# Kernel optimization log

Hardware: AMD Instinct MI355X
Metric: run time of the kernel (lower is better)

## Reference

```python
import jax, jax.numpy as jnp
import numpy as np

N, E, G = 50000, 600000, 50
IN_CH, HID, OUT, HEADS = 5, 64, 32, 4
BN_EPS = 1e-5


def setup_inputs() -> dict:
    key = jax.random.key(0)
    ks = jax.random.split(key, 32)

    def p(i, shape, scale=0.1):
        return jax.random.normal(ks[i], shape, dtype=jnp.float32) * scale

    inp = {
        "x": jax.random.normal(ks[0], (N, IN_CH), dtype=jnp.float32),
        "edge_index": jax.random.randint(ks[1], (2, E), 0, N),
        "batch": jnp.sort(jax.random.randint(ks[2], (N,), 0, G)),
        "enc_w": p(3, (IN_CH, HID)),
        "enc_b": jnp.zeros((HID,), jnp.float32),
    }
    dims = [(HID, HID), (HID, HID), (HID, OUT)]
    i = 4
    for l, (din, dout) in enumerate(dims):
        inp[f"w{l}"] = p(i, (din, HEADS * dout)); i += 1
        inp[f"as{l}"] = p(i, (HEADS, dout)); i += 1
        inp[f"ad{l}"] = p(i, (HEADS, dout)); i += 1
        inp[f"b{l}"] = jnp.zeros((dout,), jnp.float32)
        inp[f"g{l}"] = jnp.ones((dout,), jnp.float32)
        inp[f"be{l}"] = jnp.zeros((dout,), jnp.float32)
    for name in ("eth", "man"):
        inp[f"{name}_w1"] = p(i, (OUT, OUT // 2)); i += 1
        inp[f"{name}_b1"] = jnp.zeros((OUT // 2,), jnp.float32)
        inp[f"{name}_w2"] = p(i, (OUT // 2, 1)); i += 1
        inp[f"{name}_b2"] = jnp.zeros((1,), jnp.float32)
    return inp


def _gat(h_in, src, dst, W, a_s, a_d, bias, dout):
    # PyG GATConv, heads=HEADS, concat=False (mean over heads)
    h = (h_in @ W).reshape(N, HEADS, dout)          # [N,H,C]
    es = (h * a_s).sum(-1)                          # [N,H] src attention term
    ed = (h * a_d).sum(-1)                          # [N,H] dst attention term
    e = jax.nn.leaky_relu(es[src] + ed[dst], 0.2)   # [E,H]
    m = jax.ops.segment_max(e, dst, num_segments=N)
    ex = jnp.exp(e - m[dst])
    s = jax.ops.segment_sum(ex, dst, num_segments=N)
    alpha = ex / (s[dst] + 1e-16)                   # edge softmax per dst
    out = jax.ops.segment_sum(h[src] * alpha[..., None], dst, num_segments=N)
    return out.mean(axis=1) + bias                  # mean over heads + bias


def _bn(x, g, b):  # BatchNorm1d with batch statistics
    mu = x.mean(0)
    var = x.var(0)
    return g * (x - mu) * jax.lax.rsqrt(var + BN_EPS) + b


def _head(g, w1, b1, w2, b2):
    return jax.nn.sigmoid(jax.nn.relu(g @ w1 + b1) @ w2 + b2)


def reference(x, edge_index, batch, enc_w, enc_b,
              w0, as0, ad0, b0, g0, be0,
              w1, as1, ad1, b1, g1, be1,
              w2, as2, ad2, b2, g2, be2,
              eth_w1, eth_b1, eth_w2, eth_b2,
              man_w1, man_b1, man_w2, man_b2):
    loops = jnp.arange(N)
    src = jnp.concatenate([edge_index[0], loops])
    dst = jnp.concatenate([edge_index[1], loops])

    h = x @ enc_w + enc_b
    layers = [(w0, as0, ad0, b0, g0, be0, HID),
              (w1, as1, ad1, b1, g1, be1, HID),
              (w2, as2, ad2, b2, g2, be2, OUT)]
    for i, (W, a_s, a_d, bias, gm, bt, dout) in enumerate(layers):
        h = _gat(h, src, dst, W, a_s, a_d, bias, dout)
        h = _bn(h, gm, bt)
        if i < len(layers) - 1:
            h = jax.nn.relu(h)  # dropout is identity at inference

    ones = jnp.ones((N,), h.dtype)
    counts = jax.ops.segment_sum(ones, batch, num_segments=G)  # [G]
    gsum = jax.ops.segment_sum(h, batch, num_segments=G)
    gmean = gsum / jnp.maximum(counts, 1.0)[:, None]
    gmax = jax.ops.segment_max(h, batch, num_segments=G)
    gmax = jnp.where(counts[:, None] > 0, gmax, 0.0)
    gemb = (gmean + gmax + gsum) / 3.0

    ethics = _head(gemb, eth_w1, eth_b1, eth_w2, eth_b2)
    manip = _head(gemb, man_w1, man_b1, man_w2, man_b2)
    return h, gemb, ethics, manip
```

## Files before the change

### kernel.cpp

```cpp
#include <hip/hip_runtime.h>
#include <math.h>

constexpr int kN  = 50000;
constexpr int kE  = 600000;
constexpr int kET = 650000;
constexpr int kG  = 50;
constexpr int kH  = 4;

constexpr size_t OFF_HCUR   = 0;
constexpr size_t OFF_HNEXT  = 1600000;
constexpr size_t OFF_Z      = 4800000;
constexpr size_t OFF_ES     = 11200000;
constexpr size_t OFF_ED     = 11400000;
constexpr size_t OFF_ROWPTR = 14200000;
constexpr size_t OFF_CURSOR = 14260000;
constexpr size_t OFF_SRC    = 14320000;
constexpr size_t OFF_WT2    = 14970000;
constexpr size_t OFF_AHAT   = 15000000;
constexpr size_t OFF_BN     = 15002000;
constexpr size_t OFF_GPOOL  = 15003000;
constexpr size_t OFF_SPART  = 15008000;

constexpr int kScanBlocks = (kN + 1023) / 1024;

typedef __bf16 bf16x8 __attribute__((ext_vector_type(8)));
typedef float  f32x4  __attribute__((ext_vector_type(4)));

__device__ inline ushort f2b(float f) {
    unsigned u = __float_as_uint(f);
    return (ushort)((u + 0x7FFFu + ((u >> 16) & 1u)) >> 16);
}
__device__ inline float b2f(ushort u) {
    return __uint_as_float(((unsigned)u) << 16);
}
__device__ inline unsigned enc_f(float f) {
    unsigned b = __float_as_uint(f);
    return (b & 0x80000000u) ? ~b : (b | 0x80000000u);
}
__device__ inline float dec_f(unsigned u) {
    return __uint_as_float((u & 0x80000000u) ? (u & 0x7FFFFFFFu) : ~u);
}

__device__ inline void edge_pair(const int* __restrict__ ei, int e, int& src, int& dst) {
    if (e < kE) { src = ei[e]; dst = ei[kE + e]; }
    else        { src = e - kE; dst = e - kE; }
}

__global__ void k_hist(const int* __restrict__ ei, int* __restrict__ counts) {
    int e = blockIdx.x * blockDim.x + threadIdx.x;
    if (e >= kET) return;
    int src, dst;
    edge_pair(ei, e, src, dst);
    atomicAdd(&counts[dst], 1);
}

__global__ void __launch_bounds__(1024) k_scan_local(const int* __restrict__ counts,
                                                     int* __restrict__ rowptr,
                                                     int* __restrict__ partials) {
    int tid = threadIdx.x;
    int idx = blockIdx.x * 1024 + tid;
    int val = (idx < kN) ? counts[idx] : 0;
    int lane = tid & 63, w = tid >> 6;
    int x = val;
#pragma unroll
    for (int off = 1; off < 64; off <<= 1) {
        int t = __shfl_up(x, off);
        if (lane >= off) x += t;
    }
    __shared__ int wsum[16];
    if (lane == 63) wsum[w] = x;
    __syncthreads();
    if (w == 0 && lane < 16) {
        int y = wsum[lane];
#pragma unroll
        for (int off = 1; off < 16; off <<= 1) {
            int t = __shfl_up(y, off);
            if (lane >= off) y += t;
        }
        wsum[lane] = y;
    }
    __syncthreads();
    int incl = x + (w > 0 ? wsum[w - 1] : 0);
    if (idx < kN) rowptr[idx + 1] = incl;
    if (tid == 1023) partials[blockIdx.x] = incl;
}

__global__ void k_scan_part(int* __restrict__ partials) {
    int lane = threadIdx.x;
    int v = (lane < kScanBlocks) ? partials[lane] : 0;
    int x = v;
#pragma unroll
    for (int off = 1; off < 64; off <<= 1) {
        int t = __shfl_up(x, off);
        if (lane >= off) x += t;
    }
    if (lane < kScanBlocks) partials[lane] = x - v;
}

__global__ void __launch_bounds__(1024) k_scan_add(int* __restrict__ cursor,
                                                   int* __restrict__ rowptr,
                                                   const int* __restrict__ partials) {
    int idx = blockIdx.x * 1024 + threadIdx.x;
    if (idx >= kN) return;
    int incl = rowptr[idx + 1] + partials[blockIdx.x];
    rowptr[idx + 1] = incl;
    int val = cursor[idx];
    cursor[idx] = incl - val;
    if (idx == 0) rowptr[0] = 0;
}

__global__ void k_scatter(const int* __restrict__ ei, int* __restrict__ cursor,
                          int* __restrict__ src_csr) {
    int e = blockIdx.x * blockDim.x + threadIdx.x;
    if (e >= kET) return;
    int src, dst;
    edge_pair(ei, e, src, dst);
    int pos = atomicAdd(&cursor[dst], 1);
    src_csr[pos] = src;
}

__global__ void k_prep_all(const float* __restrict__ w0, const float* __restrict__ w1,
                           const float* __restrict__ w2, const float* __restrict__ as0,
                           const float* __restrict__ as1, const float* __restrict__ as2,
                           const float* __restrict__ ad0, const float* __restrict__ ad1,
                           const float* __restrict__ ad2, float* __restrict__ ahat,
                           ushort* __restrict__ Wt2) {
    int b = blockIdx.x;
    if (b < 3) {
        const float* W  = (b == 0) ? w0 : (b == 1) ? w1 : w2;
        const float* As = (b == 0) ? as0 : (b == 1) ? as1 : as2;
        const float* Ad = (b == 0) ? ad0 : (b == 1) ? ad1 : ad2;
        int dout = (b == 2) ? 32 : 64;
        int i = threadIdx.x;
        int h = i >> 6, k = i & 63;
        const float* wr = W + (size_t)k * (4 * dout) + h * dout;
        float s1 = 0.f, s2 = 0.f;
        for (int c = 0; c < dout; ++c) {
            float w = wr[c];
            s1 += w * As[h * dout + c];
            s2 += w * Ad[h * dout + c];
        }
        ahat[b * 512 + i] = s1;
        ahat[b * 512 + 256 + i] = s2;
    } else {
        int i = (b - 3) * 256 + threadIdx.x;
        if (i >= 40960) return;
        int l, li;
        if (i < 16384)      { l = 0; li = i; }
        else if (i < 32768) { l = 1; li = i - 16384; }
        else                { l = 2; li = i - 32768; }
        int dout = (l == 2) ? 32 : 64;
        const float* W = (l == 0) ? w0 : (l == 1) ? w1 : w2;
        int c = li >> 8, kk = li & 255;
        int h = kk >> 6, k = kk & 63;
        Wt2[l * 16384 + li] = f2b(W[(size_t)k * (4 * dout) + h * dout + c]);
    }
}

__global__ void __launch_bounds__(256) k_encoder_att(const float* __restrict__ x,
                                                     const float* __restrict__ w,
                                                     const float* __restrict__ b,
                                                     const float* __restrict__ ahat0,
                                                     ushort* __restrict__ h,
                                                     float* __restrict__ es,
                                                     float* __restrict__ ed) {
    int node = blockIdx.x * 4 + (threadIdx.x >> 6);
    int lane = threadIdx.x & 63;
    float acc = b[lane];
#pragma unroll
    for (int k = 0; k < 5; ++k) acc += x[node * 5 + k] * w[k * 64 + lane];
    h[(size_t)node * 64 + lane] = f2b(acc);

    float ps[4], pd[4];
#pragma unroll
    for (int hh = 0; hh < 4; ++hh) {
        ps[hh] = acc * ahat0[hh * 64 + lane];
        pd[hh] = acc * ahat0[256 + hh * 64 + lane];
    }
#pragma unroll
    for (int off = 1; off < 64; off <<= 1) {
#pragma unroll
        for (int hh = 0; hh < 4; ++hh) {
            ps[hh] += __shfl_xor(ps[hh], off);
            pd[hh] += __shfl_xor(pd[hh], off);
        }
    }
    if (lane == 0) {
        ((float4*)es)[node] = make_float4(ps[0], ps[1], ps[2], ps[3]);
        ((float4*)ed)[node] = make_float4(pd[0], pd[1], pd[2], pd[3]);
    }
}

__global__ void __launch_bounds__(256) k_gat(const int* __restrict__ rowptr,
                                             const int* __restrict__ srcc,
                                             const float* __restrict__ es,
                                             const float* __restrict__ ed,
                                             const ushort* __restrict__ h,
                                             ushort* __restrict__ z) {
    int wid = threadIdx.x >> 6;
    int lane = threadIdx.x & 63;
    int dst = blockIdx.x * 4 + wid;
    int start = rowptr[dst], end = rowptr[dst + 1];
    int deg = end - start;

    int e_l = lane >> 2, hh = lane & 3;
    int q = lane >> 4, c4 = lane & 15;

    float edv = ed[dst * 4 + hh];
    float acc[4][4] = {};
    float s;

    if (deg <= 16) {
        int pos = start + e_l;
        int psafe = (pos < end) ? pos : start;
        int src = srcc[psafe];
        float v = es[src * 4 + hh] + edv;
        v = (v >= 0.f) ? v : 0.2f * v;
        if (pos >= end) v = -3e38f;

        uint2 hv[4];
#pragma unroll
        for (int t = 0; t < 4; ++t) {
            int p2 = start + t * 4 + q;
            int p2s = (p2 < end) ? p2 : start;
            int s2 = srcc[p2s];
            hv[t] = *reinterpret_cast<const uint2*>(h + (size_t)s2 * 64 + c4 * 4);
        }

        float cm = v;
        cm = fmaxf(cm, __shfl_xor(cm, 4));
        cm = fmaxf(cm, __shfl_xor(cm, 8));
        cm = fmaxf(cm, __shfl_xor(cm, 16));
        cm = fmaxf(cm, __shfl_xor(cm, 32));
        float p = __expf(v - cm);
        float cs = p;
        cs += __shfl_xor(cs, 4);
        cs += __shfl_xor(cs, 8);
        cs += __shfl_xor(cs, 16);
        cs += __shfl_xor(cs, 32);
        s = cs;

#pragma unroll
        for (int t = 0; t < 4; ++t) {
            int el = t * 4 + q;
            float p0 = __shfl(p, (el << 2) | 0);
            float p1 = __shfl(p, (el << 2) | 1);
            float p2 = __shfl(p, (el << 2) | 2);
            float p3 = __shfl(p, (el << 2) | 3);
            float c0 = __uint_as_float(hv[t].x << 16);
            float c1 = __uint_as_float(hv[t].x & 0xFFFF0000u);
            float c2 = __uint_as_float(hv[t].y << 16);
            float c3 = __uint_as_float(hv[t].y & 0xFFFF0000u);
            acc[0][0] += p0 * c0; acc[0][1] += p0 * c1; acc[0][2] += p0 * c2; acc[0][3] += p0 * c3;
            acc[1][0] += p1 * c0; acc[1][1] += p1 * c1; acc[1][2] += p1 * c2; acc[1][3] += p1 * c3;
            acc[2][0] += p2 * c0; acc[2][1] += p2 * c1; acc[2][2] += p2 * c2; acc[2][3] += p2 * c3;
            acc[3][0] += p3 * c0; acc[3][1] += p3 * c1; acc[3][2] += p3 * c2; acc[3][3] += p3 * c3;
        }
    } else {
        float m = -3e38f;
        s = 0.f;
        for (int cs0 = start; cs0 < end; cs0 += 16) {
            int pos = cs0 + e_l;
            int psafe = (pos < end) ? pos : start;
            int src = srcc[psafe];
            float v = es[src * 4 + hh] + edv;
            v = (v >= 0.f) ? v : 0.2f * v;
            if (pos >= end) v = -3e38f;

            float cm = v;
            cm = fmaxf(cm, __shfl_xor(cm, 4));
            cm = fmaxf(cm, __shfl_xor(cm, 8));
            cm = fmaxf(cm, __shfl_xor(cm, 16));
            cm = fmaxf(cm, __shfl_xor(cm, 32));
            float mn = fmaxf(m, cm);
            float scale = __expf(m - mn);
            float p = __expf(v - mn);
            float cth = p;
            cth += __shfl_xor(cth, 4);
            cth += __shfl_xor(cth, 8);
            cth += __shfl_xor(cth, 16);
            cth += __shfl_xor(cth, 32);
            s = s * scale + cth;
            m = mn;

            float sc0 = __shfl(scale, 0), sc1 = __shfl(scale, 1);
            float sc2 = __shfl(scale, 2), sc3 = __shfl(scale, 3);
#pragma unroll
            for (int c = 0; c < 4; ++c) {
                acc[0][c] *= sc0; acc[1][c] *= sc1; acc[2][c] *= sc2; acc[3][c] *= sc3;
            }
#pragma unroll
            for (int t = 0; t < 4; ++t) {
                int el = t * 4 + q;
                int p2 = cs0 + el;
                int p2s = (p2 < end) ? p2 : start;
                int s2 = srcc[p2s];
                uint2 hv = *reinterpret_cast<const uint2*>(h + (size_t)s2 * 64 + c4 * 4);
                float p0 = __shfl(p, (el << 2) | 0);
                float p1 = __shfl(p, (el << 2) | 1);
                float p2f = __shfl(p, (el << 2) | 2);
                float p3 = __shfl(p, (el << 2) | 3);
                float c0 = __uint_as_float(hv.x << 16);
                float c1 = __uint_as_float(hv.x & 0xFFFF0000u);
                float c2 = __uint_as_float(hv.y << 16);
                float c3 = __uint_as_float(hv.y & 0xFFFF0000u);
                acc[0][0] += p0 * c0;  acc[0][1] += p0 * c1;  acc[0][2] += p0 * c2;  acc[0][3] += p0 * c3;
                acc[1][0] += p1 * c0;  acc[1][1] += p1 * c1;  acc[1][2] += p1 * c2;  acc[1][3] += p1 * c3;
                acc[2][0] += p2f * c0; acc[2][1] += p2f * c1; acc[2][2] += p2f * c2; acc[2][3] += p2f * c3;
                acc[3][0] += p3 * c0;  acc[3][1] += p3 * c1;  acc[3][2] += p3 * c2;  acc[3][3] += p3 * c3;
            }
        }
    }

    float myinv = 0.25f / (s + 1e-16f);
    float inv0 = __shfl(myinv, 0), inv1 = __shfl(myinv, 1);
    float inv2 = __shfl(myinv, 2), inv3 = __shfl(myinv, 3);
#pragma unroll
    for (int c = 0; c < 4; ++c) {
        acc[0][c] *= inv0; acc[1][c] *= inv1; acc[2][c] *= inv2; acc[3][c] *= inv3;
    }
#pragma unroll
    for (int j = 0; j < 4; ++j) {
#pragma unroll
        for (int c = 0; c < 4; ++c) {
            float v = acc[j][c];
            v += __shfl_xor(v, 16);
            v += __shfl_xor(v, 32);
            acc[j][c] = v;
        }
    }
    if (q == 0) {
        ushort* zr = z + (size_t)dst * 256 + c4 * 4;
#pragma unroll
        for (int j = 0; j < 4; ++j) {
            ushort4 o;
            o.x = f2b(acc[j][0]); o.y = f2b(acc[j][1]);
            o.z = f2b(acc[j][2]); o.w = f2b(acc[j][3]);
            *reinterpret_cast<ushort4*>(zr + j * 64) = o;
        }
    }
}

template <int DOUT>
__global__ void __launch_bounds__(256) k_zgemm(const ushort* __restrict__ z,
                                               const ushort* __restrict__ Wt2l,
                                               float* __restrict__ hnext,
                                               float* __restrict__ bnl) {
    constexpr int NG = DOUT / 32;
    constexpr int W = 2 * DOUT;
    __shared__ float pl[4][W];
    int tid = threadIdx.x;
    int widx = tid >> 6, lane = tid & 63;
    int wid = blockIdx.x * 4 + widx;
    int mtile = wid / NG;
    int ng = wid - mtile * NG;
    bool active = (mtile < kN / 16);
    int m0 = mtile * 16;
    int n0 = ng * 32;

    int row = lane & 15;
    int k0  = (lane >> 4) * 8;

    for (int j = tid; j < 4 * W; j += 256) (&pl[0][0])[j] = 0.f;

    f32x4 acc0 = {0.f, 0.f, 0.f, 0.f};
    f32x4 acc1 = {0.f, 0.f, 0.f, 0.f};
    if (active) {
        const ushort* za = z + (size_t)(m0 + row) * 256 + k0;
        bf16x8 a[8];
#pragma unroll
        for (int ks = 0; ks < 8; ++ks)
            a[ks] = *reinterpret_cast<const bf16x8*>(za + ks * 32);

        const ushort* wb0 = Wt2l + (size_t)(n0 + row) * 256 + k0;
        const ushort* wb1 = wb0 + 16 * 256;
#pragma unroll
        for (int ks = 0; ks < 8; ++ks) {
            bf16x8 b0 = *reinterpret_cast<const bf16x8*>(wb0 + ks * 32);
            bf16x8 b1 = *reinterpret_cast<const bf16x8*>(wb1 + ks * 32);
            acc0 = __builtin_amdgcn_mfma_f32_16x16x32_bf16(a[ks], b0, acc0, 0, 0, 0);
            acc1 = __builtin_amdgcn_mfma_f32_16x16x32_bf16(a[ks], b1, acc1, 0, 0, 0);
        }

        int col = lane & 15;
        int r0  = (lane >> 4) * 4;
#pragma unroll
        for (int r = 0; r < 4; ++r) {
            hnext[(size_t)(m0 + r0 + r) * DOUT + n0 + col]      = acc0[r];
            hnext[(size_t)(m0 + r0 + r) * DOUT + n0 + 16 + col] = acc1[r];
        }
    }

    float s0 = 0.f, q0 = 0.f, s1 = 0.f, q1 = 0.f;
#pragma unroll
    for (int r = 0; r < 4; ++r) {
        s0 += acc0[r]; q0 += acc0[r] * acc0[r];
        s1 += acc1[r]; q1 += acc1[r] * acc1[r];
    }
    s0 += __shfl_xor(s0, 16); s0 += __shfl_xor(s0, 32);
    q0 += __shfl_xor(q0, 16); q0 += __shfl_xor(q0, 32);
    s1 += __shfl_xor(s1, 16); s1 += __shfl_xor(s1, 32);
    q1 += __shfl_xor(q1, 16); q1 += __shfl_xor(q1, 32);
    __syncthreads();
    if (lane < 16) {
        pl[widx][n0 + lane]             = s0;
        pl[widx][DOUT + n0 + lane]      = q0;
        pl[widx][n0 + 16 + lane]        = s1;
        pl[widx][DOUT + n0 + 16 + lane] = q1;
    }
    __syncthreads();
    if (tid < W) {
        float t = pl[0][tid] + pl[1][tid] + pl[2][tid] + pl[3][tid];
        atomicAdd(&bnl[tid], t);
    }
}

__global__ void __launch_bounds__(256) k_bn_apply_att(const float* __restrict__ hnext,
                                                      const float* __restrict__ bn,
                                                      const float* __restrict__ g,
                                                      const float* __restrict__ be,
                                                      const float* __restrict__ ahat_next,
                                                      ushort* __restrict__ hcur,
                                                      float* __restrict__ es,
                                                      float* __restrict__ ed) {
    int node = blockIdx.x * 4 + (threadIdx.x >> 6);
    int lane = threadIdx.x & 63;
    float mu = bn[lane] * (1.f / kN);
    float var = bn[64 + lane] * (1.f / kN) - mu * mu;
    float v = g[lane] * (hnext[(size_t)node * 64 + lane] - mu) * rsqrtf(var + 1e-5f) + be[lane];
    v = fmaxf(v, 0.f);
    hcur[(size_t)node * 64 + lane] = f2b(v);

    float ps[4], pd[4];
#pragma unroll
    for (int hh = 0; hh < 4; ++hh) {
        ps[hh] = v * ahat_next[hh * 64 + lane];
        pd[hh] = v * ahat_next[256 + hh * 64 + lane];
    }
#pragma unroll
    for (int off = 1; off < 64; off <<= 1) {
#pragma unroll
        for (int hh = 0; hh < 4; ++hh) {
            ps[hh] += __shfl_xor(ps[hh], off);
            pd[hh] += __shfl_xor(pd[hh], off);
        }
    }
    if (lane == 0) {
        ((float4*)es)[node] = make_float4(ps[0], ps[1], ps[2], ps[3]);
        ((float4*)ed)[node] = make_float4(pd[0], pd[1], pd[2], pd[3]);
    }
}

__global__ void __launch_bounds__(256) k_bn_apply32_pool(const float* __restrict__ hnext,
                                                         const float* __restrict__ bn,
                                                         const float* __restrict__ g,
                                                         const float* __restrict__ be,
                                                         const int* __restrict__ batch,
                                                         float* __restrict__ out_h,
                                                         float* __restrict__ gsum,
                                                         unsigned* __restrict__ gmaxe) {
    int tid = threadIdx.x;
    int i = blockIdx.x * 256 + tid;
    int n = i >> 5, c = i & 31;
    float mu = bn[c] * (1.f / kN);
    float var = bn[32 + c] * (1.f / kN) - mu * mu;
    float v = g[c] * (hnext[i] - mu) * rsqrtf(var + 1e-5f) + be[c];
    out_h[i] = v;

    __shared__ float ls[256];
    ls[tid] = v;
    __syncthreads();
    int nb0 = blockIdx.x * 8;
    int gfirst = batch[nb0], glast = batch[nb0 + 7];
    if (gfirst == glast) {
        if (tid < 32) {
            float s = 0.f;
            unsigned me = 0u;
#pragma unroll
            for (int r = 0; r < 8; ++r) {
                float vv = ls[r * 32 + tid];
                s += vv;
                unsigned e = enc_f(vv);
                me = (e > me) ? e : me;
            }
            atomicAdd(&gsum[gfirst * 32 + tid], s);
            atomicMax(&gmaxe[gfirst * 32 + tid], me);
        }
    } else {
        int gg = batch[n];
        atomicAdd(&gsum[gg * 32 + c], v);
        atomicMax(&gmaxe[gg * 32 + c], enc_f(v));
    }
}

__global__ void __launch_bounds__(256) k_finish(const float* __restrict__ gsum,
                                                const unsigned* __restrict__ gmaxe,
                                                const int* __restrict__ batch,
                                                const float* __restrict__ ew1,
                                                const float* __restrict__ eb1,
                                                const float* __restrict__ ew2,
                                                const float* __restrict__ eb2,
                                                const float* __restrict__ mw1,
                                                const float* __restrict__ mb1,
                                                const float* __restrict__ mw2,
                                                const float* __restrict__ mb2,
                                                float* __restrict__ out_gemb,
                                                float* __restrict__ out_eth,
                                                float* __restrict__ out_man) {
    __shared__ int bound[kG + 1];
    __shared__ float ge[kG * 32];
    int tid = threadIdx.x;
    if (tid <= kG) {
        int lo = 0, hi = kN;
        while (lo < hi) { int mid = (lo + hi) >> 1; if (batch[mid] < tid) lo = mid + 1; else hi = mid; }
        bound[tid] = lo;
    }
    __syncthreads();
    for (int j = tid; j < kG * 32; j += 256) {
        int gg = j >> 5;
        int cnt = bound[gg + 1] - bound[gg];
        float sum = gsum[j];
        float mx = (cnt > 0) ? dec_f(gmaxe[j]) : 0.f;
        float mean = sum / fmaxf((float)cnt, 1.f);
        float e = (mean + mx + sum) * (1.f / 3.f);
        ge[j] = e;
        out_gemb[j] = e;
    }
    __syncthreads();
    if (tid < kG) {
        const float* row = &ge[tid * 32];
        float acc_e = eb2[0], acc_m = mb2[0];
#pragma unroll 4
        for (int j = 0; j < 16; ++j) {
            float he = eb1[j], hm = mb1[j];
            for (int k = 0; k < 32; ++k) {
                float v = row[k];
                he += v * ew1[k * 16 + j];
                hm += v * mw1[k * 16 + j];
            }
            acc_e += fmaxf(he, 0.f) * ew2[j];
            acc_m += fmaxf(hm, 0.f) * mw2[j];
        }
        out_eth[tid] = 1.f / (1.f + expf(-acc_e));
        out_man[tid] = 1.f / (1.f + expf(-acc_m));
    }
}

extern "C" void kernel_launch(void* const* d_in, const int* in_sizes, int n_in,
                              void* d_out, int out_size, void* d_ws, size_t ws_size,
                              hipStream_t stream) {
    const float* x     = (const float*)d_in[0];
    const int*   ei    = (const int*)d_in[1];
    const int*   batch = (const int*)d_in[2];
    const float* enc_w = (const float*)d_in[3];
    const float* enc_b = (const float*)d_in[4];

    float* ws = (float*)d_ws;
    ushort*   hcur  = (ushort*)(ws + OFF_HCUR);
    float*    hnext = ws + OFF_HNEXT;
    ushort*   z     = (ushort*)(ws + OFF_Z);
    float*    es    = ws + OFF_ES;
    float*    ed    = ws + OFF_ED;
    int*      rowptr= (int*)(ws + OFF_ROWPTR);
    int*      cursor= (int*)(ws + OFF_CURSOR);
    int*      srcc  = (int*)(ws + OFF_SRC);
    ushort*   Wt2   = (ushort*)(ws + OFF_WT2);
    float*    ahat  = ws + OFF_AHAT;
    float*    bn    = ws + OFF_BN;
    float*    gsum  = ws + OFF_GPOOL;
    unsigned* gmaxe = (unsigned*)(ws + OFF_GPOOL + 1600);
    int*      spart = (int*)(ws + OFF_SPART);

    float* out      = (float*)d_out;
    float* out_h    = out;
    float* out_gemb = out + 1600000;
    float* out_eth  = out + 1601600;
    float* out_man  = out + 1601650;

    hipMemsetAsync(cursor, 0, kN * sizeof(int), stream);
    hipMemsetAsync(ws + OFF_BN, 0, 4200 * sizeof(float), stream);

    k_hist<<<(kET + 255) / 256, 256, 0, stream>>>(ei, cursor);
    k_scan_local<<<kScanBlocks, 1024, 0, stream>>>(cursor, rowptr, spart);
    k_scan_part<<<1, 64, 0, stream>>>(spart);
    k_scan_add<<<kScanBlocks, 1024, 0, stream>>>(cursor, rowptr, spart);
    k_scatter<<<(kET + 255) / 256, 256, 0, stream>>>(ei, cursor, srcc);

    k_prep_all<<<163, 256, 0, stream>>>((const float*)d_in[5], (const float*)d_in[11],
                                        (const float*)d_in[17], (const float*)d_in[6],
                                        (const float*)d_in[12], (const float*)d_in[18],
                                        (const float*)d_in[7], (const float*)d_in[13],
                                        (const float*)d_in[19], ahat, Wt2);

    k_encoder_att<<<kN / 4, 256, 0, stream>>>(x, enc_w, enc_b, ahat, hcur, es, ed);

    for (int l = 0; l < 3; ++l) {
        const float* gam = (const float*)d_in[9 + 6 * l];
        const float* bet = (const float*)d_in[10 + 6 * l];
        const ushort* Wt2l = Wt2 + l * 16384;
        float* bnl = bn + l * 128;

        k_gat<<<kN / 4, 256, 0, stream>>>(rowptr, srcc, es, ed, hcur, z);

        if (l < 2) {
            k_zgemm<64><<<1563, 256, 0, stream>>>(z, Wt2l, hnext, bnl);
            k_bn_apply_att<<<kN / 4, 256, 0, stream>>>(hnext, bnl, gam, bet,
                                                       ahat + (l + 1) * 512, hcur, es, ed);
        } else {
            k_zgemm<32><<<782, 256, 0, stream>>>(z, Wt2l, hnext, bnl);
            k_bn_apply32_pool<<<kN * 32 / 256, 256, 0, stream>>>(hnext, bnl, gam, bet,
                                                                 batch, out_h, gsum, gmaxe);
        }
    }

    k_finish<<<1, 256, 0, stream>>>(gsum, gmaxe, batch,
                                    (const float*)d_in[23], (const float*)d_in[24],
                                    (const float*)d_in[25], (const float*)d_in[26],
                                    (const float*)d_in[27], (const float*)d_in[28],
                                    (const float*)d_in[29], (const float*)d_in[30],
                                    out_gemb, out_eth, out_man);
}
```

Baseline: 535.0 us.

## Fuse setup kernels, split zgemm tiles, and replicate BN stat accumulators

Merges the edge histogram into the weight-prep kernel and the CSR scatter into the encoder kernel, which removes launches and lets independent work share a grid. The two memsets become one contiguous memset. The z-GEMM now gives each wave a single 16-column tile instead of two, doubling the grid and dropping the shared A-fragment reuse across column tiles. BatchNorm sum and sum-of-squares atomics are spread over 16 replica buffers to cut same-address contention, and the apply kernels add the replicas back together.

```diff
diff --git a/kernel.cpp b/kernel.cpp
--- a/kernel.cpp
+++ b/kernel.cpp
@@ -6,6 +6,7 @@
 constexpr int kET = 650000;
 constexpr int kG  = 50;
 constexpr int kH  = 4;
+constexpr int kRep = 16;
 
 constexpr size_t OFF_HCUR   = 0;
 constexpr size_t OFF_HNEXT  = 1600000;
@@ -13,15 +14,19 @@
 constexpr size_t OFF_ES     = 11200000;
 constexpr size_t OFF_ED     = 11400000;
 constexpr size_t OFF_ROWPTR = 14200000;
-constexpr size_t OFF_CURSOR = 14260000;
 constexpr size_t OFF_SRC    = 14320000;
 constexpr size_t OFF_WT2    = 14970000;
 constexpr size_t OFF_AHAT   = 15000000;
-constexpr size_t OFF_BN     = 15002000;
-constexpr size_t OFF_GPOOL  = 15003000;
-constexpr size_t OFF_SPART  = 15008000;
+constexpr size_t OFF_SPART  = 15002000;
+constexpr size_t OFF_CURSOR = 15010000;
+constexpr size_t OFF_BNREP  = 15060000;
+constexpr size_t OFF_GPOOL  = 15066144;
+constexpr size_t kZeroEnd   = 15069344;
 
 constexpr int kScanBlocks = (kN + 1023) / 1024;
+constexpr int kHistBlocks = (kET + 255) / 256;
+constexpr int kPrepBlocks = 163;
+constexpr int kEncBlocks  = kN / 4;
 
 typedef __bf16 bf16x8 __attribute__((ext_vector_type(8)));
 typedef float  f32x4  __attribute__((ext_vector_type(4)));
@@ -46,80 +51,8 @@
     else        { src = e - kE; dst = e - kE; }
 }
 
-__global__ void k_hist(const int* __restrict__ ei, int* __restrict__ counts) {
-    int e = blockIdx.x * blockDim.x + threadIdx.x;
-    if (e >= kET) return;
-    int src, dst;
-    edge_pair(ei, e, src, dst);
-    atomicAdd(&counts[dst], 1);
-}
-
-__global__ void __launch_bounds__(1024) k_scan_local(const int* __restrict__ counts,
-                                                     int* __restrict__ rowptr,
-                                                     int* __restrict__ partials) {
-    int tid = threadIdx.x;
-    int idx = blockIdx.x * 1024 + tid;
-    int val = (idx < kN) ? counts[idx] : 0;
-    int lane = tid & 63, w = tid >> 6;
-    int x = val;
-#pragma unroll
-    for (int off = 1; off < 64; off <<= 1) {
-        int t = __shfl_up(x, off);
-        if (lane >= off) x += t;
-    }
-    __shared__ int wsum[16];
-    if (lane == 63) wsum[w] = x;
-    __syncthreads();
-    if (w == 0 && lane < 16) {
-        int y = wsum[lane];
-#pragma unroll
-        for (int off = 1; off < 16; off <<= 1) {
-            int t = __shfl_up(y, off);
-            if (lane >= off) y += t;
-        }
-        wsum[lane] = y;
-    }
-    __syncthreads();
-    int incl = x + (w > 0 ? wsum[w - 1] : 0);
-    if (idx < kN) rowptr[idx + 1] = incl;
-    if (tid == 1023) partials[blockIdx.x] = incl;
-}
-
-__global__ void k_scan_part(int* __restrict__ partials) {
-    int lane = threadIdx.x;
-    int v = (lane < kScanBlocks) ? partials[lane] : 0;
-    int x = v;
-#pragma unroll
-    for (int off = 1; off < 64; off <<= 1) {
-        int t = __shfl_up(x, off);
-        if (lane >= off) x += t;
-    }
-    if (lane < kScanBlocks) partials[lane] = x - v;
-}
-
-__global__ void __launch_bounds__(1024) k_scan_add(int* __restrict__ cursor,
-                                                   int* __restrict__ rowptr,
-                                                   const int* __restrict__ partials) {
-    int idx = blockIdx.x * 1024 + threadIdx.x;
-    if (idx >= kN) return;
-    int incl = rowptr[idx + 1] + partials[blockIdx.x];
-    rowptr[idx + 1] = incl;
-    int val = cursor[idx];
-    cursor[idx] = incl - val;
-    if (idx == 0) rowptr[0] = 0;
-}
-
-__global__ void k_scatter(const int* __restrict__ ei, int* __restrict__ cursor,
-                          int* __restrict__ src_csr) {
-    int e = blockIdx.x * blockDim.x + threadIdx.x;
-    if (e >= kET) return;
-    int src, dst;
-    edge_pair(ei, e, src, dst);
-    int pos = atomicAdd(&cursor[dst], 1);
-    src_csr[pos] = src;
-}
-
-__global__ void k_prep_all(const float* __restrict__ w0, const float* __restrict__ w1,
+__global__ void k_histprep(const int* __restrict__ ei, int* __restrict__ counts,
+                           const float* __restrict__ w0, const float* __restrict__ w1,
                            const float* __restrict__ w2, const float* __restrict__ as0,
                            const float* __restrict__ as1, const float* __restrict__ as2,
                            const float* __restrict__ ad0, const float* __restrict__ ad1,
@@ -142,7 +75,7 @@
         }
         ahat[b * 512 + i] = s1;
         ahat[b * 512 + 256 + i] = s2;
-    } else {
+    } else if (b < kPrepBlocks) {
         int i = (b - 3) * 256 + threadIdx.x;
         if (i >= 40960) return;
         int l, li;
@@ -154,40 +87,113 @@
         int c = li >> 8, kk = li & 255;
         int h = kk >> 6, k = kk & 63;
         Wt2[l * 16384 + li] = f2b(W[(size_t)k * (4 * dout) + h * dout + c]);
-    }
-}
-
-__global__ void __launch_bounds__(256) k_encoder_att(const float* __restrict__ x,
+    } else {
+        int e = (b - kPrepBlocks) * 256 + threadIdx.x;
+        if (e >= kET) return;
+        int src, dst;
+        edge_pair(ei, e, src, dst);
+        atomicAdd(&counts[dst], 1);
+    }
+}
+
+__global__ void __launch_bounds__(1024) k_scan_local(const int* __restrict__ counts,
+                                                     int* __restrict__ rowptr,
+                                                     int* __restrict__ partials) {
+    int tid = threadIdx.x;
+    int idx = blockIdx.x * 1024 + tid;
+    int val = (idx < kN) ? counts[idx] : 0;
+    int lane = tid & 63, w = tid >> 6;
+    int x = val;
+#pragma unroll
+    for (int off = 1; off < 64; off <<= 1) {
+        int t = __shfl_up(x, off);
+        if (lane >= off) x += t;
+    }
+    __shared__ int wsum[16];
+    if (lane == 63) wsum[w] = x;
+    __syncthreads();
+    if (w == 0 && lane < 16) {
+        int y = wsum[lane];
+#pragma unroll
+        for (int off = 1; off < 16; off <<= 1) {
+            int t = __shfl_up(y, off);
+            if (lane >= off) y += t;
+        }
+        wsum[lane] = y;
+    }
+    __syncthreads();
+    int incl = x + (w > 0 ? wsum[w - 1] : 0);
+    if (idx < kN) rowptr[idx + 1] = incl;
+    if (tid == 1023) partials[blockIdx.x] = incl;
+}
+
+__global__ void k_scan_part(int* __restrict__ partials) {
+    int lane = threadIdx.x;
+    int v = (lane < kScanBlocks) ? partials[lane] : 0;
+    int x = v;
+#pragma unroll
+    for (int off = 1; off < 64; off <<= 1) {
+        int t = __shfl_up(x, off);
+        if (lane >= off) x += t;
+    }
+    if (lane < kScanBlocks) partials[lane] = x - v;
+}
+
+__global__ void __launch_bounds__(1024) k_scan_add(int* __restrict__ cursor,
+                                                   int* __restrict__ rowptr,
+                                                   const int* __restrict__ partials) {
+    int idx = blockIdx.x * 1024 + threadIdx.x;
+    if (idx >= kN) return;
+    int incl = rowptr[idx + 1] + partials[blockIdx.x];
+    rowptr[idx + 1] = incl;
+    int val = cursor[idx];
+    cursor[idx] = incl - val;
+    if (idx == 0) rowptr[0] = 0;
+}
+
+__global__ void __launch_bounds__(256) k_scatter_enc(const int* __restrict__ ei,
+                                                     int* __restrict__ cursor,
+                                                     int* __restrict__ src_csr,
+                                                     const float* __restrict__ x,
                                                      const float* __restrict__ w,
                                                      const float* __restrict__ b,
                                                      const float* __restrict__ ahat0,
                                                      ushort* __restrict__ h,
                                                      float* __restrict__ es,
                                                      float* __restrict__ ed) {
-    int node = blockIdx.x * 4 + (threadIdx.x >> 6);
-    int lane = threadIdx.x & 63;
-    float acc = b[lane];
-#pragma unroll
-    for (int k = 0; k < 5; ++k) acc += x[node * 5 + k] * w[k * 64 + lane];
-    h[(size_t)node * 64 + lane] = f2b(acc);
-
-    float ps[4], pd[4];
-#pragma unroll
-    for (int hh = 0; hh < 4; ++hh) {
-        ps[hh] = acc * ahat0[hh * 64 + lane];
-        pd[hh] = acc * ahat0[256 + hh * 64 + lane];
-    }
-#pragma unroll
-    for (int off = 1; off < 64; off <<= 1) {
+    if (blockIdx.x < kEncBlocks) {
+        int node = blockIdx.x * 4 + (threadIdx.x >> 6);
+        int lane = threadIdx.x & 63;
+        float acc = b[lane];
+#pragma unroll
+        for (int k = 0; k < 5; ++k) acc += x[node * 5 + k] * w[k * 64 + lane];
+        h[(size_t)node * 64 + lane] = f2b(acc);
+
+        float ps[4], pd[4];
 #pragma unroll
         for (int hh = 0; hh < 4; ++hh) {
-            ps[hh] += __shfl_xor(ps[hh], off);
-            pd[hh] += __shfl_xor(pd[hh], off);
-        }
-    }
-    if (lane == 0) {
-        ((float4*)es)[node] = make_float4(ps[0], ps[1], ps[2], ps[3]);
-        ((float4*)ed)[node] = make_float4(pd[0], pd[1], pd[2], pd[3]);
+            ps[hh] = acc * ahat0[hh * 64 + lane];
+            pd[hh] = acc * ahat0[256 + hh * 64 + lane];
+        }
+#pragma unroll
+        for (int off = 1; off < 64; off <<= 1) {
+#pragma unroll
+            for (int hh = 0; hh < 4; ++hh) {
+                ps[hh] += __shfl_xor(ps[hh], off);
+                pd[hh] += __shfl_xor(pd[hh], off);
+            }
+        }
+        if (lane == 0) {
+            ((float4*)es)[node] = make_float4(ps[0], ps[1], ps[2], ps[3]);
+            ((float4*)ed)[node] = make_float4(pd[0], pd[1], pd[2], pd[3]);
+        }
+    } else {
+        int e = (blockIdx.x - kEncBlocks) * 256 + threadIdx.x;
+        if (e >= kET) return;
+        int src, dst;
+        edge_pair(ei, e, src, dst);
+        int pos = atomicAdd(&cursor[dst], 1);
+        src_csr[pos] = src;
     }
 }
 
@@ -345,78 +351,60 @@
 __global__ void __launch_bounds__(256) k_zgemm(const ushort* __restrict__ z,
                                                const ushort* __restrict__ Wt2l,
                                                float* __restrict__ hnext,
-                                               float* __restrict__ bnl) {
-    constexpr int NG = DOUT / 32;
+                                               float* __restrict__ bnrep_l) {
+    constexpr int NT = DOUT / 16;
     constexpr int W = 2 * DOUT;
     __shared__ float pl[4][W];
     int tid = threadIdx.x;
     int widx = tid >> 6, lane = tid & 63;
     int wid = blockIdx.x * 4 + widx;
-    int mtile = wid / NG;
-    int ng = wid - mtile * NG;
+    int mtile = wid / NT;
+    int nt = wid - mtile * NT;
     bool active = (mtile < kN / 16);
     int m0 = mtile * 16;
-    int n0 = ng * 32;
+    int n0 = nt * 16;
 
     int row = lane & 15;
     int k0  = (lane >> 4) * 8;
 
     for (int j = tid; j < 4 * W; j += 256) (&pl[0][0])[j] = 0.f;
 
-    f32x4 acc0 = {0.f, 0.f, 0.f, 0.f};
-    f32x4 acc1 = {0.f, 0.f, 0.f, 0.f};
+    f32x4 acc = {0.f, 0.f, 0.f, 0.f};
     if (active) {
         const ushort* za = z + (size_t)(m0 + row) * 256 + k0;
-        bf16x8 a[8];
-#pragma unroll
-        for (int ks = 0; ks < 8; ++ks)
-            a[ks] = *reinterpret_cast<const bf16x8*>(za + ks * 32);
-
-        const ushort* wb0 = Wt2l + (size_t)(n0 + row) * 256 + k0;
-        const ushort* wb1 = wb0 + 16 * 256;
+        const ushort* wb = Wt2l + (size_t)(n0 + row) * 256 + k0;
 #pragma unroll
         for (int ks = 0; ks < 8; ++ks) {
-            bf16x8 b0 = *reinterpret_cast<const bf16x8*>(wb0 + ks * 32);
-            bf16x8 b1 = *reinterpret_cast<const bf16x8*>(wb1 + ks * 32);
-            acc0 = __builtin_amdgcn_mfma_f32_16x16x32_bf16(a[ks], b0, acc0, 0, 0, 0);
-            acc1 = __builtin_amdgcn_mfma_f32_16x16x32_bf16(a[ks], b1, acc1, 0, 0, 0);
-        }
-
+            bf16x8 a = *reinterpret_cast<const bf16x8*>(za + ks * 32);
+            bf16x8 b = *reinterpret_cast<const bf16x8*>(wb + ks * 32);
+            acc = __builtin_amdgcn_mfma_f32_16x16x32_bf16(a, b, acc, 0, 0, 0);
+        }
         int col = lane & 15;
         int r0  = (lane >> 4) * 4;
 #pragma unroll
-        for (int r = 0; r < 4; ++r) {
-            hnext[(size_t)(m0 + r0 + r) * DOUT + n0 + col]      = acc0[r];
-            hnext[(size_t)(m0 + r0 + r) * DOUT + n0 + 16 + col] = acc1[r];
-        }
-    }
-
-    float s0 = 0.f, q0 = 0.f, s1 = 0.f, q1 = 0.f;
-#pragma unroll
-    for (int r = 0; r < 4; ++r) {
-        s0 += acc0[r]; q0 += acc0[r] * acc0[r];
-        s1 += acc1[r]; q1 += acc1[r] * acc1[r];
-    }
+        for (int r = 0; r < 4; ++r)
+            hnext[(size_t)(m0 + r0 + r) * DOUT + n0 + col] = acc[r];
+    }
+
+    float s0 = 0.f, q0 = 0.f;
+#pragma unroll
+    for (int r = 0; r < 4; ++r) { s0 += acc[r]; q0 += acc[r] * acc[r]; }
     s0 += __shfl_xor(s0, 16); s0 += __shfl_xor(s0, 32);
     q0 += __shfl_xor(q0, 16); q0 += __shfl_xor(q0, 32);
-    s1 += __shfl_xor(s1, 16); s1 += __shfl_xor(s1, 32);
-    q1 += __shfl_xor(q1, 16); q1 += __shfl_xor(q1, 32);
     __syncthreads();
     if (lane < 16) {
-        pl[widx][n0 + lane]             = s0;
-        pl[widx][DOUT + n0 + lane]      = q0;
-        pl[widx][n0 + 16 + lane]        = s1;
-        pl[widx][DOUT + n0 + 16 + lane] = q1;
+        pl[widx][n0 + lane]        = s0;
+        pl[widx][DOUT + n0 + lane] = q0;
     }
     __syncthreads();
     if (tid < W) {
         float t = pl[0][tid] + pl[1][tid] + pl[2][tid] + pl[3][tid];
-        atomicAdd(&bnl[tid], t);
+        atomicAdd(&bnrep_l[(blockIdx.x & (kRep - 1)) * 128 + tid], t);
     }
 }
 
 __global__ void __launch_bounds__(256) k_bn_apply_att(const float* __restrict__ hnext,
-                                                      const float* __restrict__ bn,
+                                                      const float* __restrict__ bnrep_l,
                                                       const float* __restrict__ g,
                                                       const float* __restrict__ be,
                                                       const float* __restrict__ ahat_next,
@@ -425,8 +413,14 @@
                                                       float* __restrict__ ed) {
     int node = blockIdx.x * 4 + (threadIdx.x >> 6);
     int lane = threadIdx.x & 63;
-    float mu = bn[lane] * (1.f / kN);
-    float var = bn[64 + lane] * (1.f / kN) - mu * mu;
+    float bs = 0.f, bq = 0.f;
+#pragma unroll
+    for (int r = 0; r < kRep; ++r) {
+        bs += bnrep_l[r * 128 + lane];
+        bq += bnrep_l[r * 128 + 64 + lane];
+    }
+    float mu = bs * (1.f / kN);
+    float var = bq * (1.f / kN) - mu * mu;
     float v = g[lane] * (hnext[(size_t)node * 64 + lane] - mu) * rsqrtf(var + 1e-5f) + be[lane];
     v = fmaxf(v, 0.f);
     hcur[(size_t)node * 64 + lane] = f2b(v);
@@ -452,7 +446,7 @@
 }
 
 __global__ void __launch_bounds__(256) k_bn_apply32_pool(const float* __restrict__ hnext,
-                                                         const float* __restrict__ bn,
+                                                         const float* __restrict__ bnrep_l,
                                                          const float* __restrict__ g,
                                                          const float* __restrict__ be,
                                                          const int* __restrict__ batch,
@@ -462,8 +456,14 @@
     int tid = threadIdx.x;
     int i = blockIdx.x * 256 + tid;
     int n = i >> 5, c = i & 31;
-    float mu = bn[c] * (1.f / kN);
-    float var = bn[32 + c] * (1.f / kN) - mu * mu;
+    float bs = 0.f, bq = 0.f;
+#pragma unroll
+    for (int r = 0; r < kRep; ++r) {
+        bs += bnrep_l[r * 128 + c];
+        bq += bnrep_l[r * 128 + 32 + c];
+    }
+    float mu = bs * (1.f / kN);
+    float var = bq * (1.f / kN) - mu * mu;
     float v = g[c] * (hnext[i] - mu) * rsqrtf(var + 1e-5f) + be[c];
     out_h[i] = v;
 
@@ -562,14 +562,14 @@
     float*    es    = ws + OFF_ES;
     float*    ed    = ws + OFF_ED;
     int*      rowptr= (int*)(ws + OFF_ROWPTR);
-    int*      cursor= (int*)(ws + OFF_CURSOR);
     int*      srcc  = (int*)(ws + OFF_SRC);
     ushort*   Wt2   = (ushort*)(ws + OFF_WT2);
     float*    ahat  = ws + OFF_AHAT;
-    float*    bn    = ws + OFF_BN;
+    int*      spart = (int*)(ws + OFF_SPART);
+    int*      cursor= (int*)(ws + OFF_CURSOR);
+    float*    bnrep = ws + OFF_BNREP;
     float*    gsum  = ws + OFF_GPOOL;
     unsigned* gmaxe = (unsigned*)(ws + OFF_GPOOL + 1600);
-    int*      spart = (int*)(ws + OFF_SPART);
 
     float* out      = (float*)d_out;
     float* out_h    = out;
@@ -577,38 +577,37 @@
     float* out_eth  = out + 1601600;
     float* out_man  = out + 1601650;
 
-    hipMemsetAsync(cursor, 0, kN * sizeof(int), stream);
-    hipMemsetAsync(ws + OFF_BN, 0, 4200 * sizeof(float), stream);
-
-    k_hist<<<(kET + 255) / 256, 256, 0, stream>>>(ei, cursor);
+    hipMemsetAsync(ws + OFF_CURSOR, 0, (kZeroEnd - OFF_CURSOR) * sizeof(float), stream);
+
+    k_histprep<<<kPrepBlocks + kHistBlocks, 256, 0, stream>>>(
+        ei, cursor,
+        (const float*)d_in[5], (const float*)d_in[11], (const float*)d_in[17],
+        (const float*)d_in[6], (const float*)d_in[12], (const float*)d_in[18],
+        (const float*)d_in[7], (const float*)d_in[13], (const float*)d_in[19],
+        ahat, Wt2);
+
     k_scan_local<<<kScanBlocks, 1024, 0, stream>>>(cursor, rowptr, spart);
     k_scan_part<<<1, 64, 0, stream>>>(spart);
     k_scan_add<<<kScanBlocks, 1024, 0, stream>>>(cursor, rowptr, spart);
-    k_scatter<<<(kET + 255) / 256, 256, 0, stream>>>(ei, cursor, srcc);
-
-    k_prep_all<<<163, 256, 0, stream>>>((const float*)d_in[5], (const float*)d_in[11],
-                                        (const float*)d_in[17], (const float*)d_in[6],
-                                        (const float*)d_in[12], (const float*)d_in[18],
-                                        (const float*)d_in[7], (const float*)d_in[13],
-                                        (const float*)d_in[19], ahat, Wt2);
-
-    k_encoder_att<<<kN / 4, 256, 0, stream>>>(x, enc_w, enc_b, ahat, hcur, es, ed);
+
+    k_scatter_enc<<<kEncBlocks + kHistBlocks, 256, 0, stream>>>(
+        ei, cursor, srcc, x, enc_w, enc_b, ahat, hcur, es, ed);
 
     for (int l = 0; l < 3; ++l) {
         const float* gam = (const float*)d_in[9 + 6 * l];
         const float* bet = (const float*)d_in[10 + 6 * l];
         const ushort* Wt2l = Wt2 + l * 16384;
-        float* bnl = bn + l * 128;
+        float* bnrep_l = bnrep + l * kRep * 128;
 
         k_gat<<<kN / 4, 256, 0, stream>>>(rowptr, srcc, es, ed, hcur, z);
 
         if (l < 2) {
-            k_zgemm<64><<<1563, 256, 0, stream>>>(z, Wt2l, hnext, bnl);
-            k_bn_apply_att<<<kN / 4, 256, 0, stream>>>(hnext, bnl, gam, bet,
+            k_zgemm<64><<<3125, 256, 0, stream>>>(z, Wt2l, hnext, bnrep_l);
+            k_bn_apply_att<<<kN / 4, 256, 0, stream>>>(hnext, bnrep_l, gam, bet,
                                                        ahat + (l + 1) * 512, hcur, es, ed);
         } else {
-            k_zgemm<32><<<782, 256, 0, stream>>>(z, Wt2l, hnext, bnl);
-            k_bn_apply32_pool<<<kN * 32 / 256, 256, 0, stream>>>(hnext, bnl, gam, bet,
+            k_zgemm<32><<<1563, 256, 0, stream>>>(z, Wt2l, hnext, bnrep_l);
+            k_bn_apply32_pool<<<kN * 32 / 256, 256, 0, stream>>>(hnext, bnrep_l, gam, bet,
                                                                  batch, out_h, gsum, gmaxe);
         }
     }
```

Result: faster. 488.0 us (-8.8%).
